# Kernel tuning notes

Measured on AMD Instinct MI355X. Metric: run time of the kernel, lower is better.

The kernel has to match this reference:

```python
import jax, jax.numpy as jnp
import numpy as np

NH, NKV, HD, RANK = 16, 4, 128, 512
DIM = NH * HD
EPS = 1.1920928955078125e-07  # torch float32 eps used by F.rms_norm default


def _rms_norm(x):
    return x * jax.lax.rsqrt(jnp.mean(x * x, axis=-1, keepdims=True) + EPS)


def _rope(x, cos, sin):
    # x: [B,H,T,HD]; cos/sin: [T,HD//2]
    h = x.shape[-1] // 2
    x1, x2 = x[..., :h], x[..., h:]
    return jnp.concatenate((x1 * cos + x2 * sin, -x1 * sin + x2 * cos), axis=-1)


def setup_inputs() -> dict:
    key = jax.random.key(0)
    ks = jax.random.split(key, 7)
    B, T = 2, 2048
    s = DIM ** -0.5
    x = jax.random.normal(ks[0], (B, T, DIM), dtype=jnp.float32)
    Wq = jax.random.normal(ks[1], (DIM, DIM), dtype=jnp.float32) * s
    Wdown = jax.random.normal(ks[2], (RANK, DIM), dtype=jnp.float32) * s
    Wkup = jax.random.normal(ks[3], (NKV * HD, RANK), dtype=jnp.float32) * s
    Wvup = jax.random.normal(ks[4], (NKV * HD, RANK), dtype=jnp.float32) * s
    Wproj = jax.random.normal(ks[5], (DIM, DIM), dtype=jnp.float32) * s
    q_gain = jnp.full((NH,), 1.0, dtype=jnp.float32)
    return {"x": x, "Wq": Wq, "Wdown": Wdown, "Wkup": Wkup, "Wvup": Wvup,
            "Wproj": Wproj, "q_gain": q_gain}


def reference(x, Wq, Wdown, Wkup, Wvup, Wproj, q_gain):
    B, T, _ = x.shape
    # q projection -> [B,NH,T,HD], rms-norm per head dim
    q = (x @ Wq.T).reshape(B, T, NH, HD).transpose(0, 2, 1, 3)
    q = _rms_norm(q)
    # low-rank latent kv
    lat = x @ Wdown.T                                   # [B,T,RANK]
    k = (lat @ Wkup.T).reshape(B, T, NKV, HD).transpose(0, 2, 1, 3)
    v = (lat @ Wvup.T).reshape(B, T, NKV, HD).transpose(0, 2, 1, 3)
    k = _rms_norm(k)
    # rotary embeddings
    inv_freq = 1.0 / (10000.0 ** (jnp.arange(0, HD, 2, dtype=jnp.float32) / HD))
    t = jnp.arange(T, dtype=jnp.float32)
    f = jnp.outer(t, inv_freq)                          # [T,HD//2]
    cos, sin = jnp.cos(f), jnp.sin(f)
    q, k = _rope(q, cos, sin), _rope(k, cos, sin)
    q = q * q_gain[None, :, None, None]
    # GQA repeat_interleave kv heads
    rep = NH // NKV
    k = jnp.repeat(k, rep, axis=1)
    v = jnp.repeat(v, rep, axis=1)
    # causal SDPA
    scores = jnp.einsum('bhqd,bhkd->bhqk', q, k) / np.sqrt(HD).astype(np.float32)
    causal = jnp.tril(jnp.ones((T, T), dtype=bool))
    scores = jnp.where(causal, scores, jnp.finfo(scores.dtype).min)
    attn = jax.nn.softmax(scores, axis=-1)
    y = jnp.einsum('bhqk,bhkd->bhqd', attn, v)          # [B,NH,T,HD]
    y = y.transpose(0, 2, 1, 3).reshape(B, T, NH * HD)
    return y @ Wproj.T
```

## Files before the change

kernel.cpp:

```cpp
#include <hip/hip_runtime.h>
#include <stdint.h>

#define B_    2
#define T_    2048
#define NH_   16
#define NKV_  4
#define HD_   128
#define RANK_ 512
#define DIM_  2048
#define BT_   (B_*T_)
#define EPS_  1.1920928955078125e-07f

typedef __bf16 bf16x8 __attribute__((ext_vector_type(8)));
typedef float  f32x4  __attribute__((ext_vector_type(4)));

__device__ inline unsigned short f2bf(float f) {
    unsigned int u = __float_as_uint(f);
    u += 0x7fff + ((u >> 16) & 1);
    return (unsigned short)(u >> 16);
}
__device__ inline float bf2f(unsigned short u) {
    return __uint_as_float(((unsigned int)u) << 16);
}

#define GLOAD_LDS16(gp, lp)                                                        \
    __builtin_amdgcn_global_load_lds(                                              \
        (const __attribute__((address_space(1))) void*)(gp),                       \
        (__attribute__((address_space(3))) void*)(lp), 16, 0, 0)

__global__ __launch_bounds__(256) void cvt_kernel(const float* __restrict__ in,
                                                  unsigned short* __restrict__ out,
                                                  int n4) {
    int i = blockIdx.x * 256 + threadIdx.x;
    if (i < n4) {
        float4 v = ((const float4*)in)[i];
        ushort4 o;
        o.x = f2bf(v.x); o.y = f2bf(v.y); o.z = f2bf(v.z); o.w = f2bf(v.w);
        ((ushort4*)out)[i] = o;
    }
}

__device__ inline void store_out(float* p, float v) { *p = v; }
__device__ inline void store_out(unsigned short* p, float v) { *p = f2bf(v); }

template <typename OT>
__global__ __launch_bounds__(256) void gemm_bt(const unsigned short* __restrict__ A,
                                               const unsigned short* __restrict__ W,
                                               OT* __restrict__ C,
                                               int M, int N, int K) {
    __shared__ unsigned short As[128][32];
    __shared__ unsigned short Ws[128][32];
    int tid  = threadIdx.x;
    int lane = tid & 63, wave = tid >> 6;
    int quad = lane >> 4, l16 = lane & 15;
    int wm = (wave >> 1) * 64, wn = (wave & 1) * 64;
    long m0 = (long)blockIdx.y * 128, n0 = (long)blockIdx.x * 128;

    int sr = wave * 32 + (lane >> 2);
    int scl = (lane & 3) * 8;
    const unsigned short* Ag0 = A + (m0 + sr) * K + scl;
    const unsigned short* Ag1 = A + (m0 + sr + 16) * K + scl;
    const unsigned short* Wg0 = W + (n0 + sr) * K + scl;
    const unsigned short* Wg1 = W + (n0 + sr + 16) * K + scl;
    unsigned short* Al0 = &As[wave * 32][0];
    unsigned short* Al1 = &As[wave * 32 + 16][0];
    unsigned short* Wl0 = &Ws[wave * 32][0];
    unsigned short* Wl1 = &Ws[wave * 32 + 16][0];

    f32x4 acc[4][4];
#pragma unroll
    for (int i = 0; i < 4; i++)
#pragma unroll
        for (int j = 0; j < 4; j++) acc[i][j] = (f32x4){0.f, 0.f, 0.f, 0.f};

    for (int k0 = 0; k0 < K; k0 += 32) {
        __syncthreads();
        GLOAD_LDS16(Ag0 + k0, Al0);
        GLOAD_LDS16(Ag1 + k0, Al1);
        GLOAD_LDS16(Wg0 + k0, Wl0);
        GLOAD_LDS16(Wg1 + k0, Wl1);
        __syncthreads();
        bf16x8 af[4], wf[4];
#pragma unroll
        for (int i = 0; i < 4; i++) af[i] = *(const bf16x8*)&As[wm + i * 16 + l16][quad * 8];
#pragma unroll
        for (int j = 0; j < 4; j++) wf[j] = *(const bf16x8*)&Ws[wn + j * 16 + l16][quad * 8];
#pragma unroll
        for (int i = 0; i < 4; i++)
#pragma unroll
            for (int j = 0; j < 4; j++)
                acc[i][j] = __builtin_amdgcn_mfma_f32_16x16x32_bf16(af[i], wf[j], acc[i][j], 0, 0, 0);
    }
#pragma unroll
    for (int i = 0; i < 4; i++)
#pragma unroll
        for (int j = 0; j < 4; j++)
#pragma unroll
            for (int r = 0; r < 4; r++) {
                long row = m0 + wm + i * 16 + quad * 4 + r;
                long col = n0 + wn + j * 16 + l16;
                store_out(&C[row * N + col], acc[i][j][r]);
            }
}

template <int NHEADS, bool GAIN>
__global__ __launch_bounds__(256) void qk_prep(const float* __restrict__ lin,
                                               const float* __restrict__ gain,
                                               unsigned short* __restrict__ out,
                                               int incols) {
    int r    = blockIdx.x * 4 + (threadIdx.x >> 6);
    int lane = threadIdx.x & 63;
    int bt = r / NHEADS, h = r % NHEADS;
    const float* ip = lin + (long)bt * incols + h * 128;
    float x1 = ip[lane], x2 = ip[lane + 64];
    float ss = x1 * x1 + x2 * x2;
#pragma unroll
    for (int off = 32; off; off >>= 1) ss += __shfl_xor(ss, off);
    float inv = rsqrtf(ss * (1.0f / 128.0f) + EPS_);
    x1 *= inv; x2 *= inv;
    int b = bt / T_, t = bt % T_;
    float freq = expf(-(float)lane * 0.14391156463f);
    float f = (float)t * freq;
    float s, c;
    sincosf(f, &s, &c);
    float g = GAIN ? gain[h] * 0.08838834764831845f : 1.0f;
    float o1 = (x1 * c + x2 * s) * g;
    float o2 = (x2 * c - x1 * s) * g;
    unsigned short* op = out + ((long)(b * NHEADS + h) * T_ + t) * 128;
    op[lane]      = f2bf(o1);
    op[lane + 64] = f2bf(o2);
}

__global__ __launch_bounds__(256) void v_transpose(const float* __restrict__ vlin,
                                                   unsigned short* __restrict__ vt) {
    __shared__ float tile[32][33];
    int bkv = blockIdx.z, b = bkv >> 2, kv = bkv & 3;
    int t0 = blockIdx.x * 32, d0 = blockIdx.y * 32;
    int tx = threadIdx.x & 31, ty = threadIdx.x >> 5;
#pragma unroll
    for (int rr = 0; rr < 32; rr += 8) {
        int t = t0 + ty + rr;
        tile[ty + rr][tx] = vlin[((long)(b * T_ + t)) * 1024 + 512 + kv * 128 + d0 + tx];
    }
    __syncthreads();
#pragma unroll
    for (int rr = 0; rr < 32; rr += 8) {
        int d = d0 + ty + rr;
        vt[((long)((b * NKV_ + kv) * 128 + d)) * T_ + t0 + tx] = f2bf(tile[tx][ty + rr]);
    }
}

__global__ __launch_bounds__(256, 3) void attn_kernel(const unsigned short* __restrict__ Q,
                                                      const unsigned short* __restrict__ Km,
                                                      const unsigned short* __restrict__ Vt,
                                                      unsigned short* __restrict__ po,
                                                      float* __restrict__ pm,
                                                      float* __restrict__ pl) {
    __shared__ alignas(16) unsigned short Ks2[4][64][32];
    __shared__ alignas(16) unsigned short Vs2[2][128][32];
    __shared__ alignas(16) unsigned short Pt[4][32][72];

    int tid = threadIdx.x, lane = tid & 63, wave = tid >> 6;
    int quad = lane >> 4, l16 = lane & 15;

    int bh  = blockIdx.x / 40;
    int rem = blockIdx.x % 40;
    int g, loc;
    if      (rem <  4) { g = 0; loc = rem;      }
    else if (rem < 12) { g = 1; loc = rem - 4;  }
    else if (rem < 24) { g = 2; loc = rem - 12; }
    else               { g = 3; loc = rem - 24; }
    int qb = g * 4 + loc / (g + 1);
    int c  = loc % (g + 1);
    int b = bh >> 4, h = bh & 15, kv = h >> 2;
    int Q0 = qb * 128 + wave * 32;

    int kt0 = c * 8;
    int nt  = min(kt0 * 8 + 64, (2 * qb + 2) * 8) / 8 - kt0;
    nt = min(8, 2 * qb + 2 - kt0);

    const unsigned short* qp = Q + ((long)(b * NH_ + h) * T_ + Q0) * 128;
    const char* kb = (const char*)(Km + (long)(b * NKV_ + kv) * T_ * 128);
    const char* vb = (const char*)(Vt + (long)(b * NKV_ + kv) * 128 * (long)T_);
    char* ksB = (char*)&Ks2[0][0][0];
    char* vsB = (char*)&Vs2[0][0][0];
    unsigned short* PtW = &Pt[wave][0][0];

    bf16x8 Qf[2][4];
#pragma unroll
    for (int u = 0; u < 2; u++)
#pragma unroll
        for (int s = 0; s < 4; s++)
            Qf[u][s] = *(const bf16x8*)&qp[(u * 16 + l16) * 128 + s * 32 + quad * 8];

    f32x4 Ot[8][2];
#pragma unroll
    for (int n = 0; n < 8; n++)
#pragma unroll
        for (int u = 0; u < 2; u++) Ot[n][u] = (f32x4){0.f, 0.f, 0.f, 0.f};
    float mr[2] = {-3.0e38f, -3.0e38f}, ls[2] = {0.f, 0.f};

    for (int kt = kt0; kt < kt0 + nt; kt++) {
        int tb = kt * 64;
        __syncthreads();
        {
            const char* kg = kb + (long)tb * 256 + wave * 64 + (lane >> 2) * 256 + (lane & 3) * 16;
            char* kl = ksB + wave * 4096 + lane * 16;
#pragma unroll
            for (int r = 0; r < 4; r++)
                GLOAD_LDS16(kg + r * 4096, kl + r * 1024);
        }
        {
            int hh = wave >> 1;
            int D0 = (wave & 1) * 64;
            const char* vg = vb + (long)(D0 + (lane >> 3) * 0) * 0;
#pragma unroll
            for (int r = 0; r < 4; r++) {
                int D = D0 + r * 16;
                const char* vgr = vb + (long)(D + (lane >> 2)) * 4096 + (long)tb * 2 + hh * 64 + (lane & 3) * 16;
                char* vl = vsB + hh * 8192 + D * 64 + lane * 16;
                GLOAD_LDS16(vgr, vl);
            }
        }
        __syncthreads();

        f32x4 sc[4][2];
#pragma unroll
        for (int j = 0; j < 4; j++)
#pragma unroll
            for (int u = 0; u < 2; u++) sc[j][u] = (f32x4){0.f, 0.f, 0.f, 0.f};
#pragma unroll
        for (int j = 0; j < 4; j++)
#pragma unroll
            for (int s = 0; s < 4; s++) {
                bf16x8 kf = *(const bf16x8*)&Ks2[s][j * 16 + l16][quad * 8];
                sc[j][0] = __builtin_amdgcn_mfma_f32_16x16x32_bf16(kf, Qf[0][s], sc[j][0], 0, 0, 0);
                sc[j][1] = __builtin_amdgcn_mfma_f32_16x16x32_bf16(kf, Qf[1][s], sc[j][1], 0, 0, 0);
            }

#pragma unroll
        for (int u = 0; u < 2; u++) {
            if (tb + 63 > Q0 + u * 16) {
                int qg = Q0 + u * 16 + l16;
#pragma unroll
                for (int j = 0; j < 4; j++)
#pragma unroll
                    for (int r = 0; r < 4; r++) {
                        int kvg = tb + j * 16 + quad * 4 + r;
                        if (kvg > qg) sc[j][u][r] = -3.0e38f;
                    }
            }
            float mx = -3.0e38f;
#pragma unroll
            for (int j = 0; j < 4; j++)
#pragma unroll
                for (int r = 0; r < 4; r++) mx = fmaxf(mx, sc[j][u][r]);
            mx = fmaxf(mx, __shfl_xor(mx, 16));
            mx = fmaxf(mx, __shfl_xor(mx, 32));
            float mnew  = fmaxf(mr[u], mx);
            float alpha = __expf(mr[u] - mnew);
            float ps = 0.f;
#pragma unroll
            for (int j = 0; j < 4; j++) {
                ushort4 pk;
                float p0 = __expf(sc[j][u][0] - mnew);
                float p1 = __expf(sc[j][u][1] - mnew);
                float p2 = __expf(sc[j][u][2] - mnew);
                float p3 = __expf(sc[j][u][3] - mnew);
                ps += (p0 + p1) + (p2 + p3);
                pk.x = f2bf(p0); pk.y = f2bf(p1); pk.z = f2bf(p2); pk.w = f2bf(p3);
                *(ushort4*)&PtW[(u * 16 + l16) * 72 + j * 16 + quad * 4] = pk;
            }
            ps += __shfl_xor(ps, 16);
            ps += __shfl_xor(ps, 32);
            ls[u] = ls[u] * alpha + ps;
            mr[u] = mnew;
#pragma unroll
            for (int n = 0; n < 8; n++) Ot[n][u] *= alpha;
        }
        __threadfence_block();

#pragma unroll
        for (int hh = 0; hh < 2; hh++) {
            bf16x8 pf0 = *(const bf16x8*)&PtW[(0 * 16 + l16) * 72 + hh * 32 + quad * 8];
            bf16x8 pf1 = *(const bf16x8*)&PtW[(1 * 16 + l16) * 72 + hh * 32 + quad * 8];
#pragma unroll
            for (int n = 0; n < 8; n++) {
                bf16x8 vf = *(const bf16x8*)&Vs2[hh][n * 16 + l16][quad * 8];
                Ot[n][0] = __builtin_amdgcn_mfma_f32_16x16x32_bf16(vf, pf0, Ot[n][0], 0, 0, 0);
                Ot[n][1] = __builtin_amdgcn_mfma_f32_16x16x32_bf16(vf, pf1, Ot[n][1], 0, 0, 0);
            }
        }
    }

    int i2 = qb * 4 + wave;
    long slot = (long)bh * 160 + 8 * g * (g + 1) + (long)(i2 & 15) * (g + 1) + c;
#pragma unroll
    for (int half = 0; half < 2; half++) {
        __threadfence_block();
#pragma unroll
        for (int n2 = 0; n2 < 4; n2++) {
            int n = half * 4 + n2;
#pragma unroll
            for (int u = 0; u < 2; u++) {
                ushort4 pk;
                pk.x = f2bf(Ot[n][u][0]); pk.y = f2bf(Ot[n][u][1]);
                pk.z = f2bf(Ot[n][u][2]); pk.w = f2bf(Ot[n][u][3]);
                *(ushort4*)&PtW[(u * 16 + l16) * 72 + n2 * 16 + quad * 4] = pk;
            }
        }
        __threadfence_block();
#pragma unroll
        for (int rr = 0; rr < 4; rr++) {
            int qrow = rr * 8 + (lane >> 3);
            int colseg = (lane & 7) * 8;
            uint4 val = *(const uint4*)&PtW[qrow * 72 + colseg];
            *(uint4*)&po[slot * 4096 + qrow * 128 + half * 64 + colseg] = val;
        }
    }
    if (lane < 16) {
        pm[slot * 32 + lane]      = mr[0];
        pm[slot * 32 + 16 + lane] = mr[1];
        pl[slot * 32 + lane]      = ls[0];
        pl[slot * 32 + 16 + lane] = ls[1];
    }
}

__global__ __launch_bounds__(256) void attn_combine(const unsigned short* __restrict__ po,
                                                    const float* __restrict__ pm,
                                                    const float* __restrict__ pl,
                                                    unsigned short* __restrict__ Y) {
    int bh = blockIdx.x >> 6, i2 = blockIdx.x & 63;
    int g = i2 >> 4, nc = g + 1;
    long slot0 = (long)bh * 160 + 8 * g * (g + 1) + (long)(i2 & 15) * nc;
    int col = threadIdx.x & 127;
    int r0  = threadIdx.x >> 7;
    int b = bh >> 4, h = bh & 15;
    for (int r = r0; r < 32; r += 2) {
        float M = -3.0e38f;
        for (int c = 0; c < nc; c++) M = fmaxf(M, pm[(slot0 + c) * 32 + r]);
        float L = 0.f, acc = 0.f;
        for (int c = 0; c < nc; c++) {
            float w = __expf(pm[(slot0 + c) * 32 + r] - M);
            L   += pl[(slot0 + c) * 32 + r] * w;
            acc += w * bf2f(po[(slot0 + c) * 4096 + r * 128 + col]);
        }
        Y[((long)b * T_ + i2 * 32 + r) * DIM_ + h * 128 + col] = f2bf(acc / L);
    }
}

extern "C" void kernel_launch(void* const* d_in, const int* in_sizes, int n_in,
                              void* d_out, int out_size, void* d_ws, size_t ws_size,
                              hipStream_t stream) {
    const float* x     = (const float*)d_in[0];
    const float* Wq    = (const float*)d_in[1];
    const float* Wdown = (const float*)d_in[2];
    const float* Wkup  = (const float*)d_in[3];
    const float* Wvup  = (const float*)d_in[4];
    const float* Wproj = (const float*)d_in[5];
    const float* qgain = (const float*)d_in[6];

    char* ws = (char*)d_ws;
    size_t off = 0;
    auto alloc = [&](size_t bytes) -> void* {
        void* p = ws + off;
        off += (bytes + 255) & ~(size_t)255;
        return p;
    };
    unsigned short* x_bf   = (unsigned short*)alloc((size_t)BT_ * DIM_ * 2);
    unsigned short* Wq_bf  = (unsigned short*)alloc((size_t)DIM_ * DIM_ * 2);
    unsigned short* Wd_bf  = (unsigned short*)alloc((size_t)RANK_ * DIM_ * 2);
    unsigned short* Wkv_bf = (unsigned short*)alloc((size_t)1024 * RANK_ * 2);
    unsigned short* Wp_bf  = (unsigned short*)alloc((size_t)DIM_ * DIM_ * 2);
    float*          q_lin  = (float*)alloc((size_t)BT_ * DIM_ * 4);
    unsigned short* lat_bf = (unsigned short*)alloc((size_t)BT_ * RANK_ * 2);
    float*          kv_lin = (float*)alloc((size_t)BT_ * 1024 * 4);
    unsigned short* q_bf   = (unsigned short*)alloc((size_t)BT_ * DIM_ * 2);
    unsigned short* k_bf   = (unsigned short*)alloc((size_t)B_ * NKV_ * T_ * 128 * 2);
    unsigned short* vT_bf  = (unsigned short*)alloc((size_t)B_ * NKV_ * T_ * 128 * 2);
    unsigned short* y_bf   = (unsigned short*)alloc((size_t)BT_ * DIM_ * 2);

    unsigned short* po = (unsigned short*)q_lin;
    float* pm = (float*)((char*)q_lin + (size_t)5120 * 4096 * 2);
    float* pl = pm + 5120 * 32;

    auto cvt = [&](const float* in, unsigned short* out, int n) {
        cvt_kernel<<<(n / 4 + 255) / 256, 256, 0, stream>>>(in, out, n / 4);
    };
    cvt(x,     x_bf,  BT_ * DIM_);
    cvt(Wq,    Wq_bf, DIM_ * DIM_);
    cvt(Wdown, Wd_bf, RANK_ * DIM_);
    cvt(Wkup,  Wkv_bf,             512 * RANK_);
    cvt(Wvup,  Wkv_bf + 512 * RANK_, 512 * RANK_);
    cvt(Wproj, Wp_bf, DIM_ * DIM_);

    gemm_bt<float><<<dim3(DIM_ / 128, BT_ / 128), 256, 0, stream>>>(x_bf, Wq_bf, q_lin, BT_, DIM_, DIM_);
    gemm_bt<unsigned short><<<dim3(RANK_ / 128, BT_ / 128), 256, 0, stream>>>(x_bf, Wd_bf, lat_bf, BT_, RANK_, DIM_);
    gemm_bt<float><<<dim3(1024 / 128, BT_ / 128), 256, 0, stream>>>(lat_bf, Wkv_bf, kv_lin, BT_, 1024, RANK_);

    qk_prep<NH_, true><<<BT_ * NH_ / 4, 256, 0, stream>>>(q_lin, qgain, q_bf, DIM_);
    qk_prep<NKV_, false><<<BT_ * NKV_ / 4, 256, 0, stream>>>(kv_lin, qgain, k_bf, 1024);
    v_transpose<<<dim3(T_ / 32, 128 / 32, B_ * NKV_), 256, 0, stream>>>(kv_lin, vT_bf);

    attn_kernel<<<dim3(32 * 40), 256, 0, stream>>>(q_bf, k_bf, vT_bf, po, pm, pl);
    attn_combine<<<dim3(32 * 64), 256, 0, stream>>>(po, pm, pl, y_bf);

    gemm_bt<float><<<dim3(DIM_ / 128, BT_ / 128), 256, 0, stream>>>(y_bf, Wp_bf, (float*)d_out, BT_, DIM_, DIM_);
}
```

Baseline: 458.9 us.

## Fuse conversions and Q/down GEMMs, store bf16 intermediates, tune attention kernel

Merges the six fp32-to-bf16 conversion launches into one kernel, and fuses the Q and Wdown projections into a single GEMM that splits its output into two buffers. Q/KV projection intermediates are now stored as bf16 instead of fp32, which halves traffic into qk_prep and v_transpose at some cost in precision before the RMS norm. The attention kernel folds log2(e) into the Q scale so it can use exp2, shares LDS between the K tile and the P buffer (adding a barrier), raises the occupancy hint to 4 blocks, and reorders blocks so heads sharing a KV group are scheduled near each other.

```diff
diff --git a/kernel.cpp b/kernel.cpp
--- a/kernel.cpp
+++ b/kernel.cpp
@@ -10,6 +10,7 @@
 #define DIM_  2048
 #define BT_   (B_*T_)
 #define EPS_  1.1920928955078125e-07f
+#define LOG2E_ 1.4426950408889634f
 
 typedef __bf16 bf16x8 __attribute__((ext_vector_type(8)));
 typedef float  f32x4  __attribute__((ext_vector_type(4)));
@@ -22,22 +23,29 @@
 __device__ inline float bf2f(unsigned short u) {
     return __uint_as_float(((unsigned int)u) << 16);
 }
+__device__ inline float fast_exp2(float x) { return __builtin_amdgcn_exp2f(x); }
 
 #define GLOAD_LDS16(gp, lp)                                                        \
     __builtin_amdgcn_global_load_lds(                                              \
         (const __attribute__((address_space(1))) void*)(gp),                       \
         (__attribute__((address_space(3))) void*)(lp), 16, 0, 0)
 
-__global__ __launch_bounds__(256) void cvt_kernel(const float* __restrict__ in,
-                                                  unsigned short* __restrict__ out,
-                                                  int n4) {
+struct CvtArgs {
+    const float* src[6];
+    unsigned short* dst[6];
+    int start4[6];
+};
+__global__ __launch_bounds__(256) void cvt_all(CvtArgs a, int total4) {
     int i = blockIdx.x * 256 + threadIdx.x;
-    if (i < n4) {
-        float4 v = ((const float4*)in)[i];
-        ushort4 o;
-        o.x = f2bf(v.x); o.y = f2bf(v.y); o.z = f2bf(v.z); o.w = f2bf(v.w);
-        ((ushort4*)out)[i] = o;
-    }
+    if (i >= total4) return;
+    int s = 0;
+#pragma unroll
+    for (int k = 1; k < 6; k++) s += (i >= a.start4[k]) ? 1 : 0;
+    int j = i - a.start4[s];
+    float4 v = ((const float4*)a.src[s])[j];
+    ushort4 o;
+    o.x = f2bf(v.x); o.y = f2bf(v.y); o.z = f2bf(v.z); o.w = f2bf(v.w);
+    ((ushort4*)a.dst[s])[j] = o;
 }
 
 __device__ inline void store_out(float* p, float v) { *p = v; }
@@ -103,16 +111,80 @@
             }
 }
 
+__global__ __launch_bounds__(256) void gemm_split(const unsigned short* __restrict__ A,
+                                                  const unsigned short* __restrict__ W,
+                                                  unsigned short* __restrict__ C1, int N1,
+                                                  unsigned short* __restrict__ C2,
+                                                  int M, int N, int K) {
+    __shared__ unsigned short As[128][32];
+    __shared__ unsigned short Ws[128][32];
+    int tid  = threadIdx.x;
+    int lane = tid & 63, wave = tid >> 6;
+    int quad = lane >> 4, l16 = lane & 15;
+    int wm = (wave >> 1) * 64, wn = (wave & 1) * 64;
+    long m0 = (long)blockIdx.y * 128, n0 = (long)blockIdx.x * 128;
+
+    int sr = wave * 32 + (lane >> 2);
+    int scl = (lane & 3) * 8;
+    const unsigned short* Ag0 = A + (m0 + sr) * K + scl;
+    const unsigned short* Ag1 = A + (m0 + sr + 16) * K + scl;
+    const unsigned short* Wg0 = W + (n0 + sr) * K + scl;
+    const unsigned short* Wg1 = W + (n0 + sr + 16) * K + scl;
+    unsigned short* Al0 = &As[wave * 32][0];
+    unsigned short* Al1 = &As[wave * 32 + 16][0];
+    unsigned short* Wl0 = &Ws[wave * 32][0];
+    unsigned short* Wl1 = &Ws[wave * 32 + 16][0];
+
+    f32x4 acc[4][4];
+#pragma unroll
+    for (int i = 0; i < 4; i++)
+#pragma unroll
+        for (int j = 0; j < 4; j++) acc[i][j] = (f32x4){0.f, 0.f, 0.f, 0.f};
+
+    for (int k0 = 0; k0 < K; k0 += 32) {
+        __syncthreads();
+        GLOAD_LDS16(Ag0 + k0, Al0);
+        GLOAD_LDS16(Ag1 + k0, Al1);
+        GLOAD_LDS16(Wg0 + k0, Wl0);
+        GLOAD_LDS16(Wg1 + k0, Wl1);
+        __syncthreads();
+        bf16x8 af[4], wf[4];
+#pragma unroll
+        for (int i = 0; i < 4; i++) af[i] = *(const bf16x8*)&As[wm + i * 16 + l16][quad * 8];
+#pragma unroll
+        for (int j = 0; j < 4; j++) wf[j] = *(const bf16x8*)&Ws[wn + j * 16 + l16][quad * 8];
+#pragma unroll
+        for (int i = 0; i < 4; i++)
+#pragma unroll
+            for (int j = 0; j < 4; j++)
+                acc[i][j] = __builtin_amdgcn_mfma_f32_16x16x32_bf16(af[i], wf[j], acc[i][j], 0, 0, 0);
+    }
+    unsigned short* Cb;
+    long ldc, nb;
+    if (n0 < N1) { Cb = C1; ldc = N1;     nb = n0; }
+    else         { Cb = C2; ldc = N - N1; nb = n0 - N1; }
+#pragma unroll
+    for (int i = 0; i < 4; i++)
+#pragma unroll
+        for (int j = 0; j < 4; j++)
+#pragma unroll
+            for (int r = 0; r < 4; r++) {
+                long row = m0 + wm + i * 16 + quad * 4 + r;
+                long col = nb + wn + j * 16 + l16;
+                Cb[row * ldc + col] = f2bf(acc[i][j][r]);
+            }
+}
+
 template <int NHEADS, bool GAIN>
-__global__ __launch_bounds__(256) void qk_prep(const float* __restrict__ lin,
+__global__ __launch_bounds__(256) void qk_prep(const unsigned short* __restrict__ lin,
                                                const float* __restrict__ gain,
                                                unsigned short* __restrict__ out,
                                                int incols) {
     int r    = blockIdx.x * 4 + (threadIdx.x >> 6);
     int lane = threadIdx.x & 63;
     int bt = r / NHEADS, h = r % NHEADS;
-    const float* ip = lin + (long)bt * incols + h * 128;
-    float x1 = ip[lane], x2 = ip[lane + 64];
+    const unsigned short* ip = lin + (long)bt * incols + h * 128;
+    float x1 = bf2f(ip[lane]), x2 = bf2f(ip[lane + 64]);
     float ss = x1 * x1 + x2 * x2;
 #pragma unroll
     for (int off = 32; off; off >>= 1) ss += __shfl_xor(ss, off);
@@ -123,7 +195,7 @@
     float f = (float)t * freq;
     float s, c;
     sincosf(f, &s, &c);
-    float g = GAIN ? gain[h] * 0.08838834764831845f : 1.0f;
+    float g = GAIN ? gain[h] * 0.08838834764831845f * LOG2E_ : 1.0f;
     float o1 = (x1 * c + x2 * s) * g;
     float o2 = (x2 * c - x1 * s) * g;
     unsigned short* op = out + ((long)(b * NHEADS + h) * T_ + t) * 128;
@@ -131,9 +203,9 @@
     op[lane + 64] = f2bf(o2);
 }
 
-__global__ __launch_bounds__(256) void v_transpose(const float* __restrict__ vlin,
+__global__ __launch_bounds__(256) void v_transpose(const unsigned short* __restrict__ vlin,
                                                    unsigned short* __restrict__ vt) {
-    __shared__ float tile[32][33];
+    __shared__ unsigned short tile[32][33];
     int bkv = blockIdx.z, b = bkv >> 2, kv = bkv & 3;
     int t0 = blockIdx.x * 32, d0 = blockIdx.y * 32;
     int tx = threadIdx.x & 31, ty = threadIdx.x >> 5;
@@ -146,25 +218,27 @@
 #pragma unroll
     for (int rr = 0; rr < 32; rr += 8) {
         int d = d0 + ty + rr;
-        vt[((long)((b * NKV_ + kv) * 128 + d)) * T_ + t0 + tx] = f2bf(tile[tx][ty + rr]);
-    }
-}
-
-__global__ __launch_bounds__(256, 3) void attn_kernel(const unsigned short* __restrict__ Q,
+        vt[((long)((b * NKV_ + kv) * 128 + d)) * T_ + t0 + tx] = tile[tx][ty + rr];
+    }
+}
+
+__global__ __launch_bounds__(256, 4) void attn_kernel(const unsigned short* __restrict__ Q,
                                                       const unsigned short* __restrict__ Km,
                                                       const unsigned short* __restrict__ Vt,
                                                       unsigned short* __restrict__ po,
                                                       float* __restrict__ pm,
                                                       float* __restrict__ pl) {
-    __shared__ alignas(16) unsigned short Ks2[4][64][32];
     __shared__ alignas(16) unsigned short Vs2[2][128][32];
-    __shared__ alignas(16) unsigned short Pt[4][32][72];
+    __shared__ alignas(16) unsigned short KsPt[4 * 32 * 72];
 
     int tid = threadIdx.x, lane = tid & 63, wave = tid >> 6;
     int quad = lane >> 4, l16 = lane & 15;
 
-    int bh  = blockIdx.x / 40;
-    int rem = blockIdx.x % 40;
+    int g8 = blockIdx.x & 7;
+    int j5 = blockIdx.x >> 3;
+    int hh = j5 / 40;
+    int rem = j5 % 40;
+    int b = g8 >> 2, kvh = g8 & 3, h = kvh * 4 + hh, bh = b * 16 + h;
     int g, loc;
     if      (rem <  4) { g = 0; loc = rem;      }
     else if (rem < 12) { g = 1; loc = rem - 4;  }
@@ -172,19 +246,17 @@
     else               { g = 3; loc = rem - 24; }
     int qb = g * 4 + loc / (g + 1);
     int c  = loc % (g + 1);
-    int b = bh >> 4, h = bh & 15, kv = h >> 2;
     int Q0 = qb * 128 + wave * 32;
 
     int kt0 = c * 8;
-    int nt  = min(kt0 * 8 + 64, (2 * qb + 2) * 8) / 8 - kt0;
-    nt = min(8, 2 * qb + 2 - kt0);
+    int nt  = min(8, 2 * qb + 2 - kt0);
 
     const unsigned short* qp = Q + ((long)(b * NH_ + h) * T_ + Q0) * 128;
-    const char* kb = (const char*)(Km + (long)(b * NKV_ + kv) * T_ * 128);
-    const char* vb = (const char*)(Vt + (long)(b * NKV_ + kv) * 128 * (long)T_);
-    char* ksB = (char*)&Ks2[0][0][0];
+    const char* kb = (const char*)(Km + (long)(b * NKV_ + kvh) * T_ * 128);
+    const char* vb = (const char*)(Vt + (long)(b * NKV_ + kvh) * 128 * (long)T_);
+    char* ksB = (char*)&KsPt[0];
     char* vsB = (char*)&Vs2[0][0][0];
-    unsigned short* PtW = &Pt[wave][0][0];
+    unsigned short* PtW = &KsPt[wave * 2304];
 
     bf16x8 Qf[2][4];
 #pragma unroll
@@ -211,14 +283,13 @@
                 GLOAD_LDS16(kg + r * 4096, kl + r * 1024);
         }
         {
-            int hh = wave >> 1;
+            int h2 = wave >> 1;
             int D0 = (wave & 1) * 64;
-            const char* vg = vb + (long)(D0 + (lane >> 3) * 0) * 0;
 #pragma unroll
             for (int r = 0; r < 4; r++) {
                 int D = D0 + r * 16;
-                const char* vgr = vb + (long)(D + (lane >> 2)) * 4096 + (long)tb * 2 + hh * 64 + (lane & 3) * 16;
-                char* vl = vsB + hh * 8192 + D * 64 + lane * 16;
+                const char* vgr = vb + (long)(D + (lane >> 2)) * 4096 + (long)tb * 2 + h2 * 64 + (lane & 3) * 16;
+                char* vl = vsB + h2 * 8192 + D * 64 + lane * 16;
                 GLOAD_LDS16(vgr, vl);
             }
         }
@@ -233,10 +304,11 @@
         for (int j = 0; j < 4; j++)
 #pragma unroll
             for (int s = 0; s < 4; s++) {
-                bf16x8 kf = *(const bf16x8*)&Ks2[s][j * 16 + l16][quad * 8];
+                bf16x8 kf = *(const bf16x8*)&KsPt[s * 2048 + (j * 16 + l16) * 32 + quad * 8];
                 sc[j][0] = __builtin_amdgcn_mfma_f32_16x16x32_bf16(kf, Qf[0][s], sc[j][0], 0, 0, 0);
                 sc[j][1] = __builtin_amdgcn_mfma_f32_16x16x32_bf16(kf, Qf[1][s], sc[j][1], 0, 0, 0);
             }
+        __syncthreads();
 
 #pragma unroll
         for (int u = 0; u < 2; u++) {
@@ -258,15 +330,15 @@
             mx = fmaxf(mx, __shfl_xor(mx, 16));
             mx = fmaxf(mx, __shfl_xor(mx, 32));
             float mnew  = fmaxf(mr[u], mx);
-            float alpha = __expf(mr[u] - mnew);
+            float alpha = fast_exp2(mr[u] - mnew);
             float ps = 0.f;
 #pragma unroll
             for (int j = 0; j < 4; j++) {
                 ushort4 pk;
-                float p0 = __expf(sc[j][u][0] - mnew);
-                float p1 = __expf(sc[j][u][1] - mnew);
-                float p2 = __expf(sc[j][u][2] - mnew);
-                float p3 = __expf(sc[j][u][3] - mnew);
+                float p0 = fast_exp2(sc[j][u][0] - mnew);
+                float p1 = fast_exp2(sc[j][u][1] - mnew);
+                float p2 = fast_exp2(sc[j][u][2] - mnew);
+                float p3 = fast_exp2(sc[j][u][3] - mnew);
                 ps += (p0 + p1) + (p2 + p3);
                 pk.x = f2bf(p0); pk.y = f2bf(p1); pk.z = f2bf(p2); pk.w = f2bf(p3);
                 *(ushort4*)&PtW[(u * 16 + l16) * 72 + j * 16 + quad * 4] = pk;
@@ -281,12 +353,12 @@
         __threadfence_block();
 
 #pragma unroll
-        for (int hh = 0; hh < 2; hh++) {
-            bf16x8 pf0 = *(const bf16x8*)&PtW[(0 * 16 + l16) * 72 + hh * 32 + quad * 8];
-            bf16x8 pf1 = *(const bf16x8*)&PtW[(1 * 16 + l16) * 72 + hh * 32 + quad * 8];
+        for (int h2 = 0; h2 < 2; h2++) {
+            bf16x8 pf0 = *(const bf16x8*)&PtW[(0 * 16 + l16) * 72 + h2 * 32 + quad * 8];
+            bf16x8 pf1 = *(const bf16x8*)&PtW[(1 * 16 + l16) * 72 + h2 * 32 + quad * 8];
 #pragma unroll
             for (int n = 0; n < 8; n++) {
-                bf16x8 vf = *(const bf16x8*)&Vs2[hh][n * 16 + l16][quad * 8];
+                bf16x8 vf = *(const bf16x8*)&Vs2[h2][n * 16 + l16][quad * 8];
                 Ot[n][0] = __builtin_amdgcn_mfma_f32_16x16x32_bf16(vf, pf0, Ot[n][0], 0, 0, 0);
                 Ot[n][1] = __builtin_amdgcn_mfma_f32_16x16x32_bf16(vf, pf1, Ot[n][1], 0, 0, 0);
             }
@@ -341,7 +413,7 @@
         for (int c = 0; c < nc; c++) M = fmaxf(M, pm[(slot0 + c) * 32 + r]);
         float L = 0.f, acc = 0.f;
         for (int c = 0; c < nc; c++) {
-            float w = __expf(pm[(slot0 + c) * 32 + r] - M);
+            float w = fast_exp2(pm[(slot0 + c) * 32 + r] - M);
             L   += pl[(slot0 + c) * 32 + r] * w;
             acc += w * bf2f(po[(slot0 + c) * 4096 + r * 128 + col]);
         }
@@ -367,36 +439,38 @@
         off += (bytes + 255) & ~(size_t)255;
         return p;
     };
-    unsigned short* x_bf   = (unsigned short*)alloc((size_t)BT_ * DIM_ * 2);
-    unsigned short* Wq_bf  = (unsigned short*)alloc((size_t)DIM_ * DIM_ * 2);
-    unsigned short* Wd_bf  = (unsigned short*)alloc((size_t)RANK_ * DIM_ * 2);
-    unsigned short* Wkv_bf = (unsigned short*)alloc((size_t)1024 * RANK_ * 2);
     unsigned short* Wp_bf  = (unsigned short*)alloc((size_t)DIM_ * DIM_ * 2);
-    float*          q_lin  = (float*)alloc((size_t)BT_ * DIM_ * 4);
-    unsigned short* lat_bf = (unsigned short*)alloc((size_t)BT_ * RANK_ * 2);
-    float*          kv_lin = (float*)alloc((size_t)BT_ * 1024 * 4);
     unsigned short* q_bf   = (unsigned short*)alloc((size_t)BT_ * DIM_ * 2);
     unsigned short* k_bf   = (unsigned short*)alloc((size_t)B_ * NKV_ * T_ * 128 * 2);
     unsigned short* vT_bf  = (unsigned short*)alloc((size_t)B_ * NKV_ * T_ * 128 * 2);
     unsigned short* y_bf   = (unsigned short*)alloc((size_t)BT_ * DIM_ * 2);
-
-    unsigned short* po = (unsigned short*)q_lin;
-    float* pm = (float*)((char*)q_lin + (size_t)5120 * 4096 * 2);
+    char* region2 = ws + off;
+    unsigned short* x_bf   = (unsigned short*)alloc((size_t)BT_ * DIM_ * 2);
+    unsigned short* Wqd_bf = (unsigned short*)alloc((size_t)2560 * DIM_ * 2);
+    unsigned short* Wkv_bf = (unsigned short*)alloc((size_t)1024 * RANK_ * 2);
+    unsigned short* q_lin  = (unsigned short*)alloc((size_t)BT_ * DIM_ * 2);
+    unsigned short* lat_bf = (unsigned short*)alloc((size_t)BT_ * RANK_ * 2);
+    unsigned short* kv_lin = (unsigned short*)alloc((size_t)BT_ * 1024 * 2);
+
+    unsigned short* po = (unsigned short*)region2;
+    float* pm = (float*)(region2 + (size_t)5120 * 4096 * 2);
     float* pl = pm + 5120 * 32;
 
-    auto cvt = [&](const float* in, unsigned short* out, int n) {
-        cvt_kernel<<<(n / 4 + 255) / 256, 256, 0, stream>>>(in, out, n / 4);
-    };
-    cvt(x,     x_bf,  BT_ * DIM_);
-    cvt(Wq,    Wq_bf, DIM_ * DIM_);
-    cvt(Wdown, Wd_bf, RANK_ * DIM_);
-    cvt(Wkup,  Wkv_bf,             512 * RANK_);
-    cvt(Wvup,  Wkv_bf + 512 * RANK_, 512 * RANK_);
-    cvt(Wproj, Wp_bf, DIM_ * DIM_);
-
-    gemm_bt<float><<<dim3(DIM_ / 128, BT_ / 128), 256, 0, stream>>>(x_bf, Wq_bf, q_lin, BT_, DIM_, DIM_);
-    gemm_bt<unsigned short><<<dim3(RANK_ / 128, BT_ / 128), 256, 0, stream>>>(x_bf, Wd_bf, lat_bf, BT_, RANK_, DIM_);
-    gemm_bt<float><<<dim3(1024 / 128, BT_ / 128), 256, 0, stream>>>(lat_bf, Wkv_bf, kv_lin, BT_, 1024, RANK_);
+    CvtArgs ca;
+    ca.src[0] = x;     ca.dst[0] = x_bf;
+    ca.src[1] = Wq;    ca.dst[1] = Wqd_bf;
+    ca.src[2] = Wdown; ca.dst[2] = Wqd_bf + (size_t)DIM_ * DIM_;
+    ca.src[3] = Wkup;  ca.dst[3] = Wkv_bf;
+    ca.src[4] = Wvup;  ca.dst[4] = Wkv_bf + (size_t)512 * RANK_;
+    ca.src[5] = Wproj; ca.dst[5] = Wp_bf;
+    int n4[6] = {BT_ * DIM_ / 4, DIM_ * DIM_ / 4, RANK_ * DIM_ / 4,
+                 512 * RANK_ / 4, 512 * RANK_ / 4, DIM_ * DIM_ / 4};
+    int acc4 = 0;
+    for (int i = 0; i < 6; i++) { ca.start4[i] = acc4; acc4 += n4[i]; }
+    cvt_all<<<(acc4 + 255) / 256, 256, 0, stream>>>(ca, acc4);
+
+    gemm_split<<<dim3(2560 / 128, BT_ / 128), 256, 0, stream>>>(x_bf, Wqd_bf, q_lin, DIM_, lat_bf, BT_, 2560, DIM_);
+    gemm_bt<unsigned short><<<dim3(1024 / 128, BT_ / 128), 256, 0, stream>>>(lat_bf, Wkv_bf, kv_lin, BT_, 1024, RANK_);
 
     qk_prep<NH_, true><<<BT_ * NH_ / 4, 256, 0, stream>>>(q_lin, qgain, q_bf, DIM_);
     qk_prep<NKV_, false><<<BT_ * NKV_ / 4, 256, 0, stream>>>(kv_lin, qgain, k_bf, 1024);
```

Result: slower. 517.2 us (+12.7%).
